# Kernel tuning notes

Hardware: AMD Instinct MI355X
Metric: run time of the kernel (lower is better)

## Reference

```python
import jax, jax.numpy as jnp
import numpy as np

DIM = 1024
HIDDEN = 3072
SCALE = 1.0 / 127.0  # fixed Q8_0-style dequant scale from QuantizedLinear


def setup_inputs() -> dict:
    key = jax.random.key(0)
    k_x, k_g, k_u, k_d = jax.random.split(key, 4)
    x = jax.random.normal(k_x, (4, 2048, DIM), dtype=jnp.float32)
    # int8-valued quantized weights stored as int32 (symmetric range like torch int8 weights)
    w_gate = jax.random.randint(k_g, (HIDDEN, DIM), -127, 128, dtype=jnp.int32)
    w_up = jax.random.randint(k_u, (HIDDEN, DIM), -127, 128, dtype=jnp.int32)
    w_down = jax.random.randint(k_d, (DIM, HIDDEN), -127, 128, dtype=jnp.int32)
    return {"x": x, "w_gate": w_gate, "w_up": w_up, "w_down": w_down}


def _dequant(w_int, dtype):
    return w_int.astype(dtype) * jnp.asarray(SCALE, dtype)


def reference(x, w_gate, w_up, w_down):
    # QuantizedLinear: dequantize int8 weight to x.dtype, then F.linear (x @ W^T)
    wg = _dequant(w_gate, x.dtype)   # [H, D]
    wu = _dequant(w_up, x.dtype)     # [H, D]
    wd = _dequant(w_down, x.dtype)   # [D, H]
    gate = jnp.einsum('bsd,hd->bsh', x, wg)
    up = jnp.einsum('bsd,hd->bsh', x, wu)
    h = jax.nn.silu(gate) * up       # SwiGLU elementwise fusion
    return jnp.einsum('bsh,dh->bsd', h, wd)
```

## Files before the change

### kernel.cpp

```cpp
#include <hip/hip_runtime.h>
#include <hip/hip_bf16.h>


typedef __attribute__((ext_vector_type(8))) __bf16 bf16x8;
typedef __attribute__((ext_vector_type(4))) float f32x4;

static constexpr float QS = 1.0f / 127.0f;

#define BAR()   asm volatile("s_barrier" ::: "memory")
#define VMCNT4() asm volatile("s_waitcnt vmcnt(4)" ::: "memory")
#define VMCNT0() asm volatile("s_waitcnt vmcnt(0)" ::: "memory")
#define PRIO1() __builtin_amdgcn_s_setprio(1)
#define PRIO0() __builtin_amdgcn_s_setprio(0)

__device__ __forceinline__ void gload_lds16(const void* g, void* l) {
  __builtin_amdgcn_global_load_lds(
      (const __attribute__((address_space(1))) void*)g,
      (__attribute__((address_space(3))) void*)l,
      16, 0, 0);
}


__global__ __launch_bounds__(256) void k_conv_x(const float* __restrict__ x,
                                                __bf16* __restrict__ xb, int n8) {
  int t = blockIdx.x * 256 + threadIdx.x;
  if (t >= n8) return;
  const float4* p = (const float4*)(x + (size_t)t * 8);
  float4 a = p[0], b = p[1];
  bf16x8 o;
  o[0] = (__bf16)a.x; o[1] = (__bf16)a.y; o[2] = (__bf16)a.z; o[3] = (__bf16)a.w;
  o[4] = (__bf16)b.x; o[5] = (__bf16)b.y; o[6] = (__bf16)b.z; o[7] = (__bf16)b.w;
  *(bf16x8*)(xb + (size_t)t * 8) = o;
}

__global__ __launch_bounds__(256) void k_conv_w1(const int* __restrict__ wg,
                                                 const int* __restrict__ wu,
                                                 __bf16* __restrict__ w1) {
  int t = blockIdx.x * 256 + threadIdx.x;
  int c8 = t & 127;
  int v = t >> 7;
  int bb = v >> 5, tt = v & 31;
  const int* src = (tt < 16) ? (wg + (size_t)(bb * 16 + tt) * 1024)
                             : (wu + (size_t)(bb * 16 + (tt & 15)) * 1024);
  const int4* p = (const int4*)(src + c8 * 8);
  int4 a = p[0], b = p[1];
  bf16x8 o;
  o[0] = (__bf16)(float)a.x; o[1] = (__bf16)(float)a.y;
  o[2] = (__bf16)(float)a.z; o[3] = (__bf16)(float)a.w;
  o[4] = (__bf16)(float)b.x; o[5] = (__bf16)(float)b.y;
  o[6] = (__bf16)(float)b.z; o[7] = (__bf16)(float)b.w;
  *(bf16x8*)(w1 + (size_t)v * 1024 + c8 * 8) = o;
}

__global__ __launch_bounds__(256) void k_conv_wd(const int* __restrict__ wdn,
                                                 __bf16* __restrict__ wdb, int n8) {
  int t = blockIdx.x * 256 + threadIdx.x;
  if (t >= n8) return;
  const int4* p = (const int4*)(wdn + (size_t)t * 8);
  int4 a = p[0], b = p[1];
  bf16x8 o;
  o[0] = (__bf16)(float)a.x; o[1] = (__bf16)(float)a.y;
  o[2] = (__bf16)(float)a.z; o[3] = (__bf16)(float)a.w;
  o[4] = (__bf16)(float)b.x; o[5] = (__bf16)(float)b.y;
  o[6] = (__bf16)(float)b.z; o[7] = (__bf16)(float)b.w;
  *(bf16x8*)(wdb + (size_t)t * 8) = o;
}


#define MFMA16(MG, NG)                                                         \
  _Pragma("unroll") for (int mi = 0; mi < 4; ++mi) {                           \
    _Pragma("unroll") for (int nj = 0; nj < 2; ++nj) {                         \
      acc[(MG)*4 + mi][(NG)*2 + nj] = __builtin_amdgcn_mfma_f32_16x16x32_bf16( \
          af[mi][0], bf[NG][nj][0], acc[(MG)*4 + mi][(NG)*2 + nj], 0, 0, 0);   \
      acc[(MG)*4 + mi][(NG)*2 + nj] = __builtin_amdgcn_mfma_f32_16x16x32_bf16( \
          af[mi][1], bf[NG][nj][1], acc[(MG)*4 + mi][(NG)*2 + nj], 0, 0, 0);   \
    }                                                                          \
  }

#define LDAF(MG)                                                               \
  _Pragma("unroll") for (int mi = 0; mi < 4; ++mi) {                           \
    af[mi][0] = *(const bf16x8*)(aL + ((MG)*64 + mi * 16 + r16) * 128 + s0);   \
    af[mi][1] = *(const bf16x8*)(aL + ((MG)*64 + mi * 16 + r16) * 128 + s1);   \
  }

#define LDBF(NG)                                                               \
  _Pragma("unroll") for (int nj = 0; nj < 2; ++nj) {                           \
    bf[NG][nj][0] = *(const bf16x8*)(bL + (bro + (NG)*32 + nj * 16) * 128 + s0); \
    bf[NG][nj][1] = *(const bf16x8*)(bL + (bro + (NG)*32 + nj * 16) * 128 + s1); \
  }

template <int MODE, int LDAK, int NT, int LDO>
__device__ __forceinline__ void gemm8_body(const __bf16* __restrict__ A,
                                           const __bf16* __restrict__ Bp,
                                           void* __restrict__ Out,
                                           int row0, int col0, int kz) {
  __shared__ __bf16 sA[2][2][128][64];
  __shared__ __bf16 sB[2][2][128][64];
  const int tid = threadIdx.x;
  const int lane = tid & 63;
  const int wid = tid >> 6;
  const int wm = wid >> 2, wn = wid & 3;
  const int r16 = lane & 15;
  const int kq = lane >> 4;

  auto STG = [&](__bf16* dst, const __bf16* src, int rbase, int kt) {
    int r0 = tid >> 3;
    int c0 = (tid & 7) ^ (r0 & 7);
    int r1 = 64 + r0;
    gload_lds16(src + (size_t)(rbase + r0) * LDAK + kt * 64 + c0 * 8,
                dst + tid * 8);
    gload_lds16(src + (size_t)(rbase + r1) * LDAK + kt * 64 + c0 * 8,
                dst + (512 + tid) * 8);
  };

  f32x4 acc[8][4] = {};

  STG(&sA[0][0][0][0], A, row0, kz);
  STG(&sB[0][0][0][0], Bp, col0, kz);
  STG(&sA[0][1][0][0], A, row0 + 128, kz);
  STG(&sB[0][1][0][0], Bp, col0 + 128, kz);
  const int kt1 = kz + (NT > 1 ? 1 : 0);
  STG(&sB[1][0][0][0], Bp, col0, kt1);
  STG(&sA[1][0][0][0], A, row0, kt1);
  VMCNT4();
  BAR();

  for (int t = 0; t < NT; ++t) {
    const int c = t & 1;
    const char* aL = (const char*)&sA[c][wm][0][0];
    const char* bL = (const char*)&sB[c][wn >> 1][0][0];
    const int bro = (wn & 1) * 64 + r16;
    const int s0 = ((kq) ^ (r16 & 7)) << 4;
    const int s1 = ((4 + kq) ^ (r16 & 7)) << 4;
    const int k1 = kz + (t + 1 < NT ? t + 1 : NT - 1);
    const int k2 = kz + (t + 2 < NT ? t + 2 : NT - 1);
    bf16x8 af[4][2], bf[2][2][2];

    LDAF(0);
    LDBF(0);
    STG(&sA[c ^ 1][1][0][0], A, row0 + 128, k1);
    BAR();
    PRIO1(); MFMA16(0, 0); PRIO0();
    BAR();
    LDBF(1);
    STG(&sB[c ^ 1][1][0][0], Bp, col0 + 128, k1);
    BAR();
    PRIO1(); MFMA16(0, 1); PRIO0();
    BAR();
    LDAF(1);
    STG(&sB[c][0][0][0], Bp, col0, k2);
    BAR();
    PRIO1(); MFMA16(1, 0); PRIO0();
    BAR();
    STG(&sA[c][0][0][0], A, row0, k2);
    BAR();
    PRIO1(); MFMA16(1, 1); PRIO0();
    VMCNT4();
    BAR();
  }

  if constexpr (MODE == 1) {
    __bf16* hout = (__bf16*)Out;
    const int hbase = (col0 + wn * 64) >> 1;
#pragma unroll
    for (int i = 0; i < 8; ++i) {
#pragma unroll
      for (int p = 0; p < 2; ++p) {
#pragma unroll
        for (int rr = 0; rr < 4; ++rr) {
          int row = row0 + wm * 128 + i * 16 + kq * 4 + rr;
          float g = acc[i][2 * p][rr] * QS;
          float u = acc[i][2 * p + 1][rr] * QS;
          float hv = (g / (1.0f + __expf(-g))) * u;
          hout[(size_t)row * LDO + hbase + p * 16 + r16] = (__bf16)hv;
        }
      }
    }
  } else {
    float* out = (float*)Out;
#pragma unroll
    for (int i = 0; i < 8; ++i)
#pragma unroll
      for (int j = 0; j < 4; ++j)
#pragma unroll
        for (int rr = 0; rr < 4; ++rr) {
          int row = row0 + wm * 128 + i * 16 + kq * 4 + rr;
          int col = col0 + wn * 64 + j * 16 + r16;
          out[(size_t)row * LDO + col] = acc[i][j][rr] * QS;
        }
  }
  VMCNT0();
}

__global__ __launch_bounds__(512, 2) void k_gemm1_8p(const __bf16* __restrict__ A,
                                                     const __bf16* __restrict__ B,
                                                     __bf16* __restrict__ H) {
  gemm8_body<1, 1024, 16, 3072>(A, B, H, blockIdx.y * 256, blockIdx.x * 256, 0);
}

__global__ __launch_bounds__(512, 2) void k_gemm2_8p(const __bf16* __restrict__ H,
                                                     const __bf16* __restrict__ B,
                                                     float* __restrict__ P) {
  int b = blockIdx.x;
  int w = (b & 7) * 32 + (b >> 3);
  int z = w >> 7;
  int rem = w & 127;
  int y = rem >> 2, x = rem & 3;
  gemm8_body<0, 3072, 24, 1024>(H, B, P + (size_t)z * (8192 * 1024),
                                y * 256, x * 256, z * 24);
}

__global__ __launch_bounds__(512, 2) void k_gemm2_8p_ns(const __bf16* __restrict__ H,
                                                        const __bf16* __restrict__ B,
                                                        float* __restrict__ O) {
  gemm8_body<0, 3072, 48, 1024>(H, B, O, blockIdx.y * 256, blockIdx.x * 256, 0);
}

__global__ __launch_bounds__(256) void k_reduce2(const float* __restrict__ p,
                                                 float* __restrict__ out, int n4) {
  int t = blockIdx.x * 256 + threadIdx.x;
  if (t >= n4) return;
  const float4* a = (const float4*)p;
  const float4* b = (const float4*)(p + (size_t)8192 * 1024);
  float4 va = a[t], vb = b[t];
  ((float4*)out)[t] = make_float4(va.x + vb.x, va.y + vb.y,
                                  va.z + vb.z, va.w + vb.w);
}


extern "C" void kernel_launch(void* const* d_in, const int* in_sizes, int n_in,
                              void* d_out, int out_size, void* d_ws, size_t ws_size,
                              hipStream_t stream) {
  const float* x = (const float*)d_in[0];
  const int* wg = (const int*)d_in[1];
  const int* wu = (const int*)d_in[2];
  const int* wd = (const int*)d_in[3];

  char* ws = (char*)d_ws;
  __bf16* xb  = (__bf16*)(ws);
  __bf16* w1  = (__bf16*)(ws + 16777216);
  __bf16* wdb = (__bf16*)(ws + 16777216 + 12582912);
  __bf16* h   = (__bf16*)(ws + 35651584);
  float*  part = (float*)(ws + 85983232);
  const bool splitk = ws_size >= (size_t)85983232 + 2u * 33554432u;

  k_conv_x<<<4096, 256, 0, stream>>>(x, xb, 1048576);
  k_conv_w1<<<3072, 256, 0, stream>>>(wg, wu, w1);
  k_conv_wd<<<1536, 256, 0, stream>>>(wd, wdb, 393216);

  k_gemm1_8p<<<dim3(24, 32), 512, 0, stream>>>(xb, w1, h);

  if (splitk) {
    k_gemm2_8p<<<256, 512, 0, stream>>>(h, wdb, part);
    k_reduce2<<<8192, 256, 0, stream>>>(part, (float*)d_out, 2097152);
  } else {
    k_gemm2_8p_ns<<<dim3(4, 32), 512, 0, stream>>>(h, wdb, (float*)d_out);
  }
}
```

Baseline: 298.5 us.

## Double-buffer register fragments to prefetch next k-tile LDS reads across MFMA phases

Restructures the GEMM main loop so A/B register fragments are ping-ponged: the next tile's first A and B fragments are read from LDS during the last MFMA phase of the current tile, and B quarter 1 is loaded ahead of the first MFMA. The global-to-LDS staging order is rotated to match, with the wait count changed from 4 to 6 in the prologue and moved earlier in the loop. The aim is to hide LDS read latency behind MFMAs. The cost is higher VGPR pressure with launch bounds of 512 threads and 2 blocks, and subtle hazards in buffer-reuse ordering.

```diff
diff --git a/kernel.cpp b/kernel.cpp
--- a/kernel.cpp
+++ b/kernel.cpp
@@ -7,11 +7,10 @@
 
 static constexpr float QS = 1.0f / 127.0f;
 
-#define BAR()   asm volatile("s_barrier" ::: "memory")
-#define VMCNT4() asm volatile("s_waitcnt vmcnt(4)" ::: "memory")
-#define VMCNT0() asm volatile("s_waitcnt vmcnt(0)" ::: "memory")
-#define PRIO1() __builtin_amdgcn_s_setprio(1)
-#define PRIO0() __builtin_amdgcn_s_setprio(0)
+#define BAR()     asm volatile("s_barrier" ::: "memory")
+#define VMCNT(N)  asm volatile("s_waitcnt vmcnt(" #N ")" ::: "memory")
+#define PRIO1()   __builtin_amdgcn_s_setprio(1)
+#define PRIO0()   __builtin_amdgcn_s_setprio(0)
 
 __device__ __forceinline__ void gload_lds16(const void* g, void* l) {
   __builtin_amdgcn_global_load_lds(
@@ -67,26 +66,26 @@
 }
 
 
-#define MFMA16(MG, NG)                                                         \
+#define MFMA16(MG, NG, AF, BF)                                                 \
   _Pragma("unroll") for (int mi = 0; mi < 4; ++mi) {                           \
     _Pragma("unroll") for (int nj = 0; nj < 2; ++nj) {                         \
       acc[(MG)*4 + mi][(NG)*2 + nj] = __builtin_amdgcn_mfma_f32_16x16x32_bf16( \
-          af[mi][0], bf[NG][nj][0], acc[(MG)*4 + mi][(NG)*2 + nj], 0, 0, 0);   \
+          AF[mi][0], BF[nj][0], acc[(MG)*4 + mi][(NG)*2 + nj], 0, 0, 0);       \
       acc[(MG)*4 + mi][(NG)*2 + nj] = __builtin_amdgcn_mfma_f32_16x16x32_bf16( \
-          af[mi][1], bf[NG][nj][1], acc[(MG)*4 + mi][(NG)*2 + nj], 0, 0, 0);   \
+          AF[mi][1], BF[nj][1], acc[(MG)*4 + mi][(NG)*2 + nj], 0, 0, 0);       \
     }                                                                          \
   }
 
-#define LDAF(MG)                                                               \
+#define LDAF2(DST, MG, AL)                                                     \
   _Pragma("unroll") for (int mi = 0; mi < 4; ++mi) {                           \
-    af[mi][0] = *(const bf16x8*)(aL + ((MG)*64 + mi * 16 + r16) * 128 + s0);   \
-    af[mi][1] = *(const bf16x8*)(aL + ((MG)*64 + mi * 16 + r16) * 128 + s1);   \
-  }
-
-#define LDBF(NG)                                                               \
+    DST[mi][0] = *(const bf16x8*)((AL) + ((MG)*64 + mi * 16 + r16) * 128 + s0);\
+    DST[mi][1] = *(const bf16x8*)((AL) + ((MG)*64 + mi * 16 + r16) * 128 + s1);\
+  }
+
+#define LDBF2(DST, NG, BL)                                                     \
   _Pragma("unroll") for (int nj = 0; nj < 2; ++nj) {                           \
-    bf[NG][nj][0] = *(const bf16x8*)(bL + (bro + (NG)*32 + nj * 16) * 128 + s0); \
-    bf[NG][nj][1] = *(const bf16x8*)(bL + (bro + (NG)*32 + nj * 16) * 128 + s1); \
+    DST[nj][0] = *(const bf16x8*)((BL) + (bro + (NG)*32 + nj * 16) * 128 + s0);\
+    DST[nj][1] = *(const bf16x8*)((BL) + (bro + (NG)*32 + nj * 16) * 128 + s1);\
   }
 
 template <int MODE, int LDAK, int NT, int LDO>
@@ -102,6 +101,9 @@
   const int wm = wid >> 2, wn = wid & 3;
   const int r16 = lane & 15;
   const int kq = lane >> 4;
+  const int bro = (wn & 1) * 64 + r16;
+  const int s0 = ((kq) ^ (r16 & 7)) << 4;
+  const int s1 = ((4 + kq) ^ (r16 & 7)) << 4;
 
   auto STG = [&](__bf16* dst, const __bf16* src, int rbase, int kt) {
     int r0 = tid >> 3;
@@ -114,48 +116,54 @@
   };
 
   f32x4 acc[8][4] = {};
-
-  STG(&sA[0][0][0][0], A, row0, kz);
-  STG(&sB[0][0][0][0], Bp, col0, kz);
-  STG(&sA[0][1][0][0], A, row0 + 128, kz);
+  bf16x8 afA[4][2], afB[4][2], bfA[2][2], bfB[2][2];
+
+  STG(&sB[0][0][0][0], Bp, col0,       kz);
   STG(&sB[0][1][0][0], Bp, col0 + 128, kz);
+  STG(&sA[0][0][0][0], A,  row0,       kz);
+  STG(&sA[0][1][0][0], A,  row0 + 128, kz);
   const int kt1 = kz + (NT > 1 ? 1 : 0);
-  STG(&sB[1][0][0][0], Bp, col0, kt1);
-  STG(&sA[1][0][0][0], A, row0, kt1);
-  VMCNT4();
+  STG(&sB[1][0][0][0], Bp, col0,       kt1);
+  STG(&sB[1][1][0][0], Bp, col0 + 128, kt1);
+  STG(&sA[1][0][0][0], A,  row0,       kt1);
+  VMCNT(6);
   BAR();
+  {
+    const char* aL = (const char*)&sA[0][wm][0][0];
+    const char* bL = (const char*)&sB[0][wn >> 1][0][0];
+    LDAF2(afA, 0, aL);
+    LDBF2(bfA, 0, bL);
+  }
 
   for (int t = 0; t < NT; ++t) {
     const int c = t & 1;
-    const char* aL = (const char*)&sA[c][wm][0][0];
-    const char* bL = (const char*)&sB[c][wn >> 1][0][0];
-    const int bro = (wn & 1) * 64 + r16;
-    const int s0 = ((kq) ^ (r16 & 7)) << 4;
-    const int s1 = ((4 + kq) ^ (r16 & 7)) << 4;
+    const char* aLc = (const char*)&sA[c][wm][0][0];
+    const char* bLc = (const char*)&sB[c][wn >> 1][0][0];
+    const char* aLn = (const char*)&sA[c ^ 1][wm][0][0];
+    const char* bLn = (const char*)&sB[c ^ 1][wn >> 1][0][0];
     const int k1 = kz + (t + 1 < NT ? t + 1 : NT - 1);
     const int k2 = kz + (t + 2 < NT ? t + 2 : NT - 1);
-    bf16x8 af[4][2], bf[2][2][2];
-
-    LDAF(0);
-    LDBF(0);
+
+    LDBF2(bfB, 1, bLc);
     STG(&sA[c ^ 1][1][0][0], A, row0 + 128, k1);
     BAR();
-    PRIO1(); MFMA16(0, 0); PRIO0();
-    BAR();
-    LDBF(1);
-    STG(&sB[c ^ 1][1][0][0], Bp, col0 + 128, k1);
-    BAR();
-    PRIO1(); MFMA16(0, 1); PRIO0();
-    BAR();
-    LDAF(1);
+    PRIO1(); MFMA16(0, 0, afA, bfA); PRIO0();
+    BAR();
+    LDAF2(afB, 1, aLc);
     STG(&sB[c][0][0][0], Bp, col0, k2);
     BAR();
-    PRIO1(); MFMA16(1, 0); PRIO0();
-    BAR();
+    PRIO1(); MFMA16(0, 1, afA, bfB); PRIO0();
+    BAR();
+    STG(&sB[c][1][0][0], Bp, col0 + 128, k2);
+    BAR();
+    PRIO1(); MFMA16(1, 0, afB, bfA); PRIO0();
+    VMCNT(4);
+    BAR();
+    LDAF2(afA, 0, aLn);
+    LDBF2(bfA, 0, bLn);
     STG(&sA[c][0][0][0], A, row0, k2);
     BAR();
-    PRIO1(); MFMA16(1, 1); PRIO0();
-    VMCNT4();
+    PRIO1(); MFMA16(1, 1, afB, bfB); PRIO0();
     BAR();
   }
 
@@ -189,7 +197,7 @@
           out[(size_t)row * LDO + col] = acc[i][j][rr] * QS;
         }
   }
-  VMCNT0();
+  VMCNT(0);
 }
 
 __global__ __launch_bounds__(512, 2) void k_gemm1_8p(const __bf16* __restrict__ A,
```

Measured after the change: 301.8 us. About the same (+1.1%).

## Replace down-projection split-K with small-tile atomic-add GEMM

Applied to the files above, without the earlier changes.

The second GEMM changes from 256x256 tiles (either split-K into a partial buffer followed by a reduce kernel, or no split) to a simple 128x128-tile, 256-thread kernel. It uses split-K of two and accumulates into the output with float atomicAdd after a memset, which removes the partial buffer and the reduce pass and launches more blocks. The new kernel is single-buffered with syncthreads between load and compute, so it loses the deep pipelining of the old body. The first GEMM also gains an lgkmcnt wait.

```diff
diff --git a/kernel.cpp b/kernel.cpp
--- a/kernel.cpp
+++ b/kernel.cpp
@@ -7,11 +7,13 @@
 
 static constexpr float QS = 1.0f / 127.0f;
 
-#define BAR()   asm volatile("s_barrier" ::: "memory")
+#define BAR()    asm volatile("s_barrier" ::: "memory")
 #define VMCNT4() asm volatile("s_waitcnt vmcnt(4)" ::: "memory")
 #define VMCNT0() asm volatile("s_waitcnt vmcnt(0)" ::: "memory")
-#define PRIO1() __builtin_amdgcn_s_setprio(1)
-#define PRIO0() __builtin_amdgcn_s_setprio(0)
+#define LGKM8()  asm volatile("s_waitcnt lgkmcnt(8)" ::: "memory")
+#define PRIO1()  __builtin_amdgcn_s_setprio(1)
+#define PRIO0()  __builtin_amdgcn_s_setprio(0)
+#define SB0()    __builtin_amdgcn_sched_barrier(0)
 
 __device__ __forceinline__ void gload_lds16(const void* g, void* l) {
   __builtin_amdgcn_global_load_lds(
@@ -89,11 +91,12 @@
     bf[NG][nj][1] = *(const bf16x8*)(bL + (bro + (NG)*32 + nj * 16) * 128 + s1); \
   }
 
-template <int MODE, int LDAK, int NT, int LDO>
-__device__ __forceinline__ void gemm8_body(const __bf16* __restrict__ A,
-                                           const __bf16* __restrict__ Bp,
-                                           void* __restrict__ Out,
-                                           int row0, int col0, int kz) {
+__global__ __launch_bounds__(512, 2) void k_gemm1_8p(const __bf16* __restrict__ A,
+                                                     const __bf16* __restrict__ Bp,
+                                                     __bf16* __restrict__ Out) {
+  constexpr int LDAK = 1024, NT = 16, LDO = 3072;
+  const int row0 = blockIdx.y * 256, col0 = blockIdx.x * 256;
+  const int kz = 0;
   __shared__ __bf16 sA[2][2][128][64];
   __shared__ __bf16 sB[2][2][128][64];
   const int tid = threadIdx.x;
@@ -119,7 +122,7 @@
   STG(&sB[0][0][0][0], Bp, col0, kz);
   STG(&sA[0][1][0][0], A, row0 + 128, kz);
   STG(&sB[0][1][0][0], Bp, col0 + 128, kz);
-  const int kt1 = kz + (NT > 1 ? 1 : 0);
+  const int kt1 = kz + 1;
   STG(&sB[1][0][0][0], Bp, col0, kt1);
   STG(&sA[1][0][0][0], A, row0, kt1);
   VMCNT4();
@@ -138,6 +141,7 @@
 
     LDAF(0);
     LDBF(0);
+    LGKM8();
     STG(&sA[c ^ 1][1][0][0], A, row0 + 128, k1);
     BAR();
     PRIO1(); MFMA16(0, 0); PRIO0();
@@ -159,72 +163,91 @@
     BAR();
   }
 
-  if constexpr (MODE == 1) {
-    __bf16* hout = (__bf16*)Out;
-    const int hbase = (col0 + wn * 64) >> 1;
-#pragma unroll
-    for (int i = 0; i < 8; ++i) {
-#pragma unroll
-      for (int p = 0; p < 2; ++p) {
-#pragma unroll
-        for (int rr = 0; rr < 4; ++rr) {
-          int row = row0 + wm * 128 + i * 16 + kq * 4 + rr;
-          float g = acc[i][2 * p][rr] * QS;
-          float u = acc[i][2 * p + 1][rr] * QS;
-          float hv = (g / (1.0f + __expf(-g))) * u;
-          hout[(size_t)row * LDO + hbase + p * 16 + r16] = (__bf16)hv;
-        }
+  __bf16* hout = Out;
+  const int hbase = (col0 + wn * 64) >> 1;
+#pragma unroll
+  for (int i = 0; i < 8; ++i) {
+#pragma unroll
+    for (int p = 0; p < 2; ++p) {
+#pragma unroll
+      for (int rr = 0; rr < 4; ++rr) {
+        int row = row0 + wm * 128 + i * 16 + kq * 4 + rr;
+        float g = acc[i][2 * p][rr] * QS;
+        float u = acc[i][2 * p + 1][rr] * QS;
+        float hv = (g / (1.0f + __expf(-g))) * u;
+        hout[(size_t)row * LDO + hbase + p * 16 + r16] = (__bf16)hv;
       }
     }
-  } else {
-    float* out = (float*)Out;
-#pragma unroll
-    for (int i = 0; i < 8; ++i)
+  }
+  VMCNT0();
+}
+
+__global__ __launch_bounds__(256) void k_gemm2a(const __bf16* __restrict__ H,
+                                                const __bf16* __restrict__ Bw,
+                                                float* __restrict__ out) {
+  __shared__ __bf16 sA[128][64];
+  __shared__ __bf16 sB[128][64];
+  const int b = blockIdx.x;
+  const int xcd = b & 7, ii = b >> 3;
+  const int z = ii >> 6;
+  const int rem = ii & 63;
+  const int yy = rem >> 3, xx = rem & 7;
+  const int row0 = (xcd * 8 + yy) * 128, col0 = xx * 128;
+  const int kz = z * 24;
+
+  const int tid = threadIdx.x;
+  const int lane = tid & 63;
+  const int wid = tid >> 6;
+  const int wm = wid >> 1, wn = wid & 1;
+  const int r16 = lane & 15;
+  const int kq = lane >> 4;
+
+  f32x4 acc[4][4] = {};
+
+  for (int kt = kz; kt < kz + 24; ++kt) {
+    __syncthreads();
+#pragma unroll
+    for (int it = 0; it < 4; ++it) {
+      int chunk = it * 256 + tid;
+      int r = chunk >> 3, kc = chunk & 7;
+      int kcs = kc ^ (r & 7);
+      gload_lds16(H + (size_t)(row0 + r) * 3072 + kt * 64 + kcs * 8,
+                  ((__bf16*)sA) + chunk * 8);
+      gload_lds16(Bw + (size_t)(col0 + r) * 3072 + kt * 64 + kcs * 8,
+                  ((__bf16*)sB) + chunk * 8);
+    }
+    __syncthreads();
+#pragma unroll
+    for (int ks = 0; ks < 2; ++ks) {
+      const int chs = ((ks * 4 + kq) ^ (r16 & 7)) << 4;
+      bf16x8 av[4], bv[4];
+#pragma unroll
+      for (int i = 0; i < 4; ++i)
+        av[i] = *(const bf16x8*)(((const char*)sA) +
+                                 (wm * 64 + i * 16 + r16) * 128 + chs);
 #pragma unroll
       for (int j = 0; j < 4; ++j)
-#pragma unroll
-        for (int rr = 0; rr < 4; ++rr) {
-          int row = row0 + wm * 128 + i * 16 + kq * 4 + rr;
-          int col = col0 + wn * 64 + j * 16 + r16;
-          out[(size_t)row * LDO + col] = acc[i][j][rr] * QS;
-        }
-  }
-  VMCNT0();
-}
-
-__global__ __launch_bounds__(512, 2) void k_gemm1_8p(const __bf16* __restrict__ A,
-                                                     const __bf16* __restrict__ B,
-                                                     __bf16* __restrict__ H) {
-  gemm8_body<1, 1024, 16, 3072>(A, B, H, blockIdx.y * 256, blockIdx.x * 256, 0);
-}
-
-__global__ __launch_bounds__(512, 2) void k_gemm2_8p(const __bf16* __restrict__ H,
-                                                     const __bf16* __restrict__ B,
-                                                     float* __restrict__ P) {
-  int b = blockIdx.x;
-  int w = (b & 7) * 32 + (b >> 3);
-  int z = w >> 7;
-  int rem = w & 127;
-  int y = rem >> 2, x = rem & 3;
-  gemm8_body<0, 3072, 24, 1024>(H, B, P + (size_t)z * (8192 * 1024),
-                                y * 256, x * 256, z * 24);
-}
-
-__global__ __launch_bounds__(512, 2) void k_gemm2_8p_ns(const __bf16* __restrict__ H,
-                                                        const __bf16* __restrict__ B,
-                                                        float* __restrict__ O) {
-  gemm8_body<0, 3072, 48, 1024>(H, B, O, blockIdx.y * 256, blockIdx.x * 256, 0);
-}
-
-__global__ __launch_bounds__(256) void k_reduce2(const float* __restrict__ p,
-                                                 float* __restrict__ out, int n4) {
-  int t = blockIdx.x * 256 + threadIdx.x;
-  if (t >= n4) return;
-  const float4* a = (const float4*)p;
-  const float4* b = (const float4*)(p + (size_t)8192 * 1024);
-  float4 va = a[t], vb = b[t];
-  ((float4*)out)[t] = make_float4(va.x + vb.x, va.y + vb.y,
-                                  va.z + vb.z, va.w + vb.w);
+        bv[j] = *(const bf16x8*)(((const char*)sB) +
+                                 (wn * 64 + j * 16 + r16) * 128 + chs);
+#pragma unroll
+      for (int i = 0; i < 4; ++i)
+#pragma unroll
+        for (int j = 0; j < 4; ++j)
+          acc[i][j] = __builtin_amdgcn_mfma_f32_16x16x32_bf16(av[i], bv[j],
+                                                              acc[i][j], 0, 0, 0);
+    }
+  }
+
+#pragma unroll
+  for (int i = 0; i < 4; ++i)
+#pragma unroll
+    for (int j = 0; j < 4; ++j)
+#pragma unroll
+      for (int r = 0; r < 4; ++r) {
+        int row = row0 + wm * 64 + i * 16 + kq * 4 + r;
+        int col = col0 + wn * 64 + j * 16 + r16;
+        atomicAdd(out + (size_t)row * 1024 + col, acc[i][j][r] * QS);
+      }
 }
 
 
@@ -241,19 +264,13 @@
   __bf16* w1  = (__bf16*)(ws + 16777216);
   __bf16* wdb = (__bf16*)(ws + 16777216 + 12582912);
   __bf16* h   = (__bf16*)(ws + 35651584);
-  float*  part = (float*)(ws + 85983232);
-  const bool splitk = ws_size >= (size_t)85983232 + 2u * 33554432u;
+
+  hipMemsetAsync(d_out, 0, (size_t)8192 * 1024 * sizeof(float), stream);
 
   k_conv_x<<<4096, 256, 0, stream>>>(x, xb, 1048576);
   k_conv_w1<<<3072, 256, 0, stream>>>(wg, wu, w1);
   k_conv_wd<<<1536, 256, 0, stream>>>(wd, wdb, 393216);
 
   k_gemm1_8p<<<dim3(24, 32), 512, 0, stream>>>(xb, w1, h);
-
-  if (splitk) {
-    k_gemm2_8p<<<256, 512, 0, stream>>>(h, wdb, part);
-    k_reduce2<<<8192, 256, 0, stream>>>(part, (float*)d_out, 2097152);
-  } else {
-    k_gemm2_8p_ns<<<dim3(4, 32), 512, 0, stream>>>(h, wdb, (float*)d_out);
-  }
-}
+  k_gemm2a<<<1024, 256, 0, stream>>>(h, wdb, (float*)d_out);
+}
```

Result: slower. 327.5 us (+9.7%).
